# Optimization experiments

Measured on AMD Instinct MI355X. Metric: run time of the kernel, lower is better.

Reference implementation:

```python
import jax, jax.numpy as jnp
import numpy as np

D_MODEL = 1024
NUM_HEADS = 16
DEPTH = D_MODEL // NUM_HEADS


def setup_inputs() -> dict:
    key = jax.random.key(0)
    ks = jax.random.split(key, 9)
    B, S = 2, 2048
    scale = 1.0 / np.sqrt(D_MODEL)
    x = jax.random.normal(ks[0], (B, S, D_MODEL), dtype=jnp.float32)
    wq = jax.random.normal(ks[1], (D_MODEL, D_MODEL), dtype=jnp.float32) * scale
    bq = jax.random.normal(ks[2], (D_MODEL,), dtype=jnp.float32) * 0.01
    wk = jax.random.normal(ks[3], (D_MODEL, D_MODEL), dtype=jnp.float32) * scale
    bk = jax.random.normal(ks[4], (D_MODEL,), dtype=jnp.float32) * 0.01
    wv = jax.random.normal(ks[5], (D_MODEL, D_MODEL), dtype=jnp.float32) * scale
    bv = jax.random.normal(ks[6], (D_MODEL,), dtype=jnp.float32) * 0.01
    wo = jax.random.normal(ks[7], (D_MODEL, D_MODEL), dtype=jnp.float32) * scale
    bo = jax.random.normal(ks[8], (D_MODEL,), dtype=jnp.float32) * 0.01
    return {"x": x, "wq": wq, "bq": bq, "wk": wk, "bk": bk,
            "wv": wv, "bv": bv, "wo": wo, "bo": bo}


def reference(x, wq, bq, wk, bk, wv, bv, wo, bo):
    B, S, _ = x.shape
    def split_heads(t):  # [B,S,D] -> [B,H,S,depth]
        return t.reshape(B, S, NUM_HEADS, DEPTH).transpose(0, 2, 1, 3)
    q = split_heads(x @ wq + bq)
    k = split_heads(x @ wk + bk)
    v = split_heads(x @ wv + bv)
    # scaled dot-product attention, full [B,H,S,S] scores as in the original
    logits = jnp.einsum('bhqd,bhkd->bhqk', q, k) / jnp.sqrt(
        jnp.asarray(DEPTH, dtype=jnp.float32))
    attn = jax.nn.softmax(logits, axis=-1)
    out = jnp.einsum('bhqk,bhkd->bhqd', attn, v)
    out = out.transpose(0, 2, 1, 3).reshape(B, S, D_MODEL)
    return out @ wo + bo
```

## Files before the change

### kernel.cpp

```cpp
#include <hip/hip_runtime.h>


#define S_LEN 2048
#define DM 1024
#define MROWS 4096
#define QSCALE 0.1803368801111244f

typedef unsigned short u16;
typedef unsigned int u32;
typedef __attribute__((ext_vector_type(8))) short short8;
typedef __attribute__((ext_vector_type(4))) float f32x4;
typedef __attribute__((ext_vector_type(4))) unsigned short u16x4;

__device__ inline float bf2f(u16 h) {
    return __uint_as_float(((u32)h) << 16);
}
__device__ inline u16 f2bf(float f) {
    u32 u = __float_as_uint(f);
    u = u + 0x7fffu + ((u >> 16) & 1u);
    return (u16)(u >> 16);
}
__device__ inline float ldin(const void* p, size_t idx, int isf32) {
    return isf32 ? ((const float*)p)[idx] : bf2f(((const u16*)p)[idx]);
}
__device__ inline void gld_lds16(const u16* g, u16* l) {
    __builtin_amdgcn_global_load_lds(
        (const __attribute__((address_space(1))) void*)g,
        (__attribute__((address_space(3))) void*)l, 16, 0, 0);
}
__device__ inline f32x4 mfma16(short8 a, short8 b, f32x4 c) {
    return __builtin_amdgcn_mfma_f32_16x16x32_bf16(a, b, c, 0, 0, 0);
}

__global__ void init_flag(int* flag) { if (threadIdx.x == 0) *flag = 0; }

__global__ void detect_f32(const u16* __restrict__ x, int* flag) {
    const int idx = blockIdx.x * 256 + threadIdx.x;
    int bad = 0;
#pragma unroll
    for (int i = 0; i < 4; i++) {
        const u16 v = x[(size_t)idx * 4 + i];
        if ((v & 0x7F80u) == 0x7F80u) bad = 1;
    }
    if (bad) atomicOr(flag, 1);
}

__global__ void prep_all(const void* __restrict__ x, u16* __restrict__ xb,
                         const void* __restrict__ wq, const void* __restrict__ wk,
                         const void* __restrict__ wv, const void* __restrict__ wo,
                         const void* __restrict__ bq, const void* __restrict__ bk,
                         const void* __restrict__ bv, const void* __restrict__ bo,
                         u16* __restrict__ wallT, u16* __restrict__ woT,
                         float* __restrict__ biasAll, float* __restrict__ biasO,
                         const int* __restrict__ flag) {
    const int f = *flag;
    const int t = threadIdx.x;
    if (blockIdx.x < 2048) {
        const size_t i8 = ((size_t)blockIdx.x * 256 + t) * 8;
        if (f) {
            const f32x4 a = ((const f32x4*)x)[i8 / 4];
            const f32x4 b = ((const f32x4*)x)[i8 / 4 + 1];
            u16 o[8];
#pragma unroll
            for (int i = 0; i < 4; i++) { o[i] = f2bf(a[i]); o[4 + i] = f2bf(b[i]); }
            *(short8*)(xb + i8) = *(const short8*)o;
        } else {
            *(short8*)(xb + i8) = ((const short8*)x)[i8 / 8];
        }
        return;
    }
    const int bid = blockIdx.x - 2048;
    if (bid == 1024) {
#pragma unroll
        for (int i = 0; i < 4; i++) {
            const int idx = i * 256 + t;
            biasAll[idx]        = ldin(bq, idx, f) * QSCALE;
            biasAll[1024 + idx] = ldin(bk, idx, f);
            biasAll[2048 + idx] = ldin(bv, idx, f);
            biasO[idx]          = ldin(bo, idx, f);
        }
        return;
    }
    __shared__ float lds[64][65];
    const int m  = bid >> 8;
    const int tk = (bid >> 4) & 15;
    const int tn = bid & 15;
    const void* src = (m == 0) ? wq : (m == 1) ? wk : (m == 2) ? wv : wo;
    const float scale = (m == 0) ? QSCALE : 1.0f;
    const int r4 = t >> 6, c = t & 63;
#pragma unroll
    for (int i = 0; i < 16; i++) {
        const int k = tk * 64 + i * 4 + r4;
        lds[i * 4 + r4][c] = ldin(src, (size_t)k * 1024 + tn * 64 + c, f);
    }
    __syncthreads();
#pragma unroll
    for (int i = 0; i < 16; i++) {
        const int n = tn * 64 + i * 4 + r4;
        const int k = tk * 64 + c;
        const u16 v = f2bf(lds[c][i * 4 + r4] * scale);
        if (m < 3) wallT[((size_t)m * 1024 + n) * 1024 + k] = v;
        else       woT[(size_t)n * 1024 + k] = v;
    }
}

__global__ __launch_bounds__(256, 2)
void gemm_qkv(const u16* __restrict__ A, const u16* __restrict__ Bt,
              const float* __restrict__ bias, u16* __restrict__ Cq,
              u16* __restrict__ Ck, u16* __restrict__ Cv,
              const int K, const int N) {
    __shared__ __align__(16) u16 As[128 * 32];
    __shared__ __align__(16) u16 Bs[128 * 32];
    const int tid = threadIdx.x;
    const int w = tid >> 6, lane = tid & 63;
    const int wm = w >> 1, wn = w & 1;
    const int l16 = lane & 15, quad = lane >> 4;
    const int tm = blockIdx.x * 128;
    const int tn = blockIdx.y * 128;
    const int region = tn >> 10;

    const int sr = w * 16 + (lane >> 2);
    const int sc = (lane & 3) * 8;
    const u16* ag0 = A + (size_t)(tm + sr) * K + sc;
    const u16* ag1 = A + (size_t)(tm + sr + 64) * K + sc;
    const u16* bg0 = Bt + (size_t)(tn + sr) * K + sc;
    const u16* bg1 = Bt + (size_t)(tn + sr + 64) * K + sc;
    u16* al = As + w * 512;
    u16* bl = Bs + w * 512;

    f32x4 acc[4][4];
#pragma unroll
    for (int i = 0; i < 4; i++)
#pragma unroll
        for (int j = 0; j < 4; j++) acc[i][j] = (f32x4){0.f, 0.f, 0.f, 0.f};

    for (int kb = 0; kb < K; kb += 32) {
        __syncthreads();
        gld_lds16(ag0 + kb, al);
        gld_lds16(ag1 + kb, al + 2048);
        gld_lds16(bg0 + kb, bl);
        gld_lds16(bg1 + kb, bl + 2048);
        __syncthreads();
        short8 af[4], bfr[4];
#pragma unroll
        for (int i = 0; i < 4; i++) {
            af[i]  = *(const short8*)(As + (wm * 64 + i * 16 + l16) * 32 + quad * 8);
            bfr[i] = *(const short8*)(Bs + (wn * 64 + i * 16 + l16) * 32 + quad * 8);
        }
#pragma unroll
        for (int i = 0; i < 4; i++)
#pragma unroll
            for (int j = 0; j < 4; j++)
                acc[i][j] = mfma16(af[i], bfr[j], acc[i][j]);
    }
#pragma unroll
    for (int j = 0; j < 4; j++) {
        const int col = tn + wn * 64 + j * 16 + l16;
        const float bv = bias[col];
#pragma unroll
        for (int i = 0; i < 4; i++) {
            const int row0 = tm + wm * 64 + i * 16 + quad * 4;
#pragma unroll
            for (int r = 0; r < 4; r++) {
                const u16 vb = f2bf(acc[i][j][r] + bv);
                const int row = row0 + r;
                if (region == 0) {
                    Cq[(size_t)row * 1024 + col] = vb;
                } else if (region == 1) {
                    const int s = row & 2047, b = row >> 11;
                    const int hd = col - 1024, h = hd >> 6, d = hd & 63;
                    Ck[(((size_t)(b * 16 + h) * 2048 + s) << 6) +
                       (((d >> 3) + s) & 7) * 8 + (d & 7)] = vb;
                } else {
                    const int s = row & 2047, b = row >> 11;
                    const int hd = col - 2048, h = hd >> 6, d = hd & 63;
                    const int sl = s & 63;
                    const int p = (sl & 32) | ((sl & 15) << 1) | ((sl >> 4) & 1);
                    const int phys = ((((p >> 3) + d) & 7) << 3) | (p & 7);
                    Cv[(((size_t)((b * 16 + h) * 32 + (s >> 6))) << 12) +
                       d * 64 + phys] = vb;
                }
            }
        }
    }
}

__global__ __launch_bounds__(256, 2)
void gemm_out64(const u16* __restrict__ A, const u16* __restrict__ Bt,
                const float* __restrict__ bias, void* __restrict__ C,
                const int K, const int N, const int* __restrict__ flag) {
    __shared__ __align__(16) u16 As[64 * 32];
    __shared__ __align__(16) u16 Bs[128 * 32];
    const int tid = threadIdx.x;
    const int w = tid >> 6, lane = tid & 63;
    const int wm = w >> 1, wn = w & 1;
    const int l16 = lane & 15, quad = lane >> 4;
    const int tm = blockIdx.x * 64;
    const int tn = blockIdx.y * 128;
    const int outf = *flag;

    const int sr = w * 16 + (lane >> 2);
    const int sc = (lane & 3) * 8;
    const u16* ag  = A + (size_t)(tm + sr) * K + sc;
    const u16* bg0 = Bt + (size_t)(tn + sr) * K + sc;
    const u16* bg1 = Bt + (size_t)(tn + sr + 64) * K + sc;
    u16* al = As + w * 512;
    u16* bl = Bs + w * 512;

    f32x4 acc[2][4];
#pragma unroll
    for (int i = 0; i < 2; i++)
#pragma unroll
        for (int j = 0; j < 4; j++) acc[i][j] = (f32x4){0.f, 0.f, 0.f, 0.f};

    for (int kb = 0; kb < K; kb += 32) {
        __syncthreads();
        gld_lds16(ag + kb, al);
        gld_lds16(bg0 + kb, bl);
        gld_lds16(bg1 + kb, bl + 2048);
        __syncthreads();
        short8 af[2], bfr[4];
#pragma unroll
        for (int i = 0; i < 2; i++)
            af[i] = *(const short8*)(As + (wm * 32 + i * 16 + l16) * 32 + quad * 8);
#pragma unroll
        for (int j = 0; j < 4; j++)
            bfr[j] = *(const short8*)(Bs + (wn * 64 + j * 16 + l16) * 32 + quad * 8);
#pragma unroll
        for (int i = 0; i < 2; i++)
#pragma unroll
            for (int j = 0; j < 4; j++)
                acc[i][j] = mfma16(af[i], bfr[j], acc[i][j]);
    }
#pragma unroll
    for (int j = 0; j < 4; j++) {
        const int col = tn + wn * 64 + j * 16 + l16;
        const float bv = bias[col];
#pragma unroll
        for (int i = 0; i < 2; i++) {
            const int row0 = tm + wm * 32 + i * 16 + quad * 4;
#pragma unroll
            for (int r = 0; r < 4; r++) {
                const float val = acc[i][j][r] + bv;
                const size_t o = (size_t)(row0 + r) * N + col;
                if (outf) ((float*)C)[o] = val;
                else      ((u16*)C)[o]   = f2bf(val);
            }
        }
    }
}

__global__ __launch_bounds__(256, 2)
void flash_attn(const u16* __restrict__ Qb, const u16* __restrict__ Ktg,
                const u16* __restrict__ Vtb, u16* __restrict__ O) {
    __shared__ __align__(16) u16 Ks[4096];
    __shared__ __align__(16) u16 Vs[4096];
    const int tid = threadIdx.x;
    const int w = tid >> 6, lane = tid & 63;
    const int l16 = lane & 15, quad = lane >> 4;
    const int bh = blockIdx.y, b = bh >> 4, h = bh & 15;
    const int q0 = blockIdx.x * 128 + w * 32;

    short8 qf[2][2];
#pragma unroll
    for (int u = 0; u < 2; u++) {
        const size_t qrow = (size_t)(b * S_LEN + q0 + u * 16 + l16) * 1024 + h * 64;
        qf[u][0] = *(const short8*)(Qb + qrow + quad * 8);
        qf[u][1] = *(const short8*)(Qb + qrow + 32 + quad * 8);
    }

    const u16* kg = Ktg + ((size_t)bh << 17) + w * 1024 + lane * 8;
    const u16* vg = Vtb + ((size_t)bh << 17) + w * 1024 + lane * 8;
    u16* kl = Ks + w * 1024;
    u16* vl = Vs + w * 1024;

    const int ka0 = l16 * 64 + ((quad + l16) & 7) * 8;
    const int ka1 = l16 * 64 + ((4 + quad + l16) & 7) * 8;

    float lsum[2] = {0.f, 0.f};
    f32x4 o[2][4];
#pragma unroll
    for (int u = 0; u < 2; u++)
#pragma unroll
        for (int d = 0; d < 4; d++) o[u][d] = (f32x4){0.f, 0.f, 0.f, 0.f};
    const f32x4 zz = (f32x4){0.f, 0.f, 0.f, 0.f};

    for (int t = 0; t < S_LEN / 64; t++) {
        __syncthreads();
        gld_lds16(kg + t * 4096,       kl);
        gld_lds16(kg + t * 4096 + 512, kl + 512);
        gld_lds16(vg + t * 4096,       vl);
        gld_lds16(vg + t * 4096 + 512, vl + 512);
        __syncthreads();

        f32x4 s[2][4];
#pragma unroll
        for (int a = 0; a < 4; a++) {
            const short8 kf0 = *(const short8*)(Ks + a * 1024 + ka0);
            const short8 kf1 = *(const short8*)(Ks + a * 1024 + ka1);
#pragma unroll
            for (int u = 0; u < 2; u++) {
                s[u][a] = mfma16(kf0, qf[u][0], zz);
                s[u][a] = mfma16(kf1, qf[u][1], s[u][a]);
            }
        }
        union { u32 u[4]; short8 s8; } pu[2][2];
#pragma unroll
        for (int u = 0; u < 2; u++) {
#pragma unroll
            for (int r = 0; r < 4; r++) {
                const float e0 = __builtin_amdgcn_exp2f(s[u][0][r]);
                const float e1 = __builtin_amdgcn_exp2f(s[u][1][r]);
                const float e2 = __builtin_amdgcn_exp2f(s[u][2][r]);
                const float e3 = __builtin_amdgcn_exp2f(s[u][3][r]);
                lsum[u] += (e0 + e1) + (e2 + e3);
                pu[u][0].u[r] = __builtin_amdgcn_perm(
                    __float_as_uint(e1), __float_as_uint(e0), 0x07060302u);
                pu[u][1].u[r] = __builtin_amdgcn_perm(
                    __float_as_uint(e3), __float_as_uint(e2), 0x07060302u);
            }
        }
#pragma unroll
        for (int dv = 0; dv < 4; dv++) {
            const short8 vf0 = *(const short8*)(Vs + dv * 1024 + ka0);
            const short8 vf1 = *(const short8*)(Vs + dv * 1024 + ka1);
#pragma unroll
            for (int u = 0; u < 2; u++) {
                o[u][dv] = mfma16(vf0, pu[u][0].s8, o[u][dv]);
                o[u][dv] = mfma16(vf1, pu[u][1].s8, o[u][dv]);
            }
        }
    }

#pragma unroll
    for (int u = 0; u < 2; u++) {
        float ssum = lsum[u];
        ssum += __shfl_xor(ssum, 16);
        ssum += __shfl_xor(ssum, 32);
        const float inv = 1.0f / ssum;
        const size_t obase =
            (size_t)(b * S_LEN + q0 + u * 16 + l16) * DM + h * 64 + quad * 4;
#pragma unroll
        for (int d = 0; d < 4; d++) {
            u16x4 pk;
#pragma unroll
            for (int r = 0; r < 4; r++) pk[r] = f2bf(o[u][d][r] * inv);
            *(u16x4*)(O + obase + d * 16) = pk;
        }
    }
}

extern "C" void kernel_launch(void* const* d_in, const int* in_sizes, int n_in,
                              void* d_out, int out_size, void* d_ws, size_t ws_size,
                              hipStream_t stream) {
    const void* x  = d_in[0];
    const void* wq = d_in[1];
    const void* bq = d_in[2];
    const void* wk = d_in[3];
    const void* bk = d_in[4];
    const void* wv = d_in[5];
    const void* bv = d_in[6];
    const void* wo = d_in[7];
    const void* bo = d_in[8];

    char* ws = (char*)d_ws;
    int*   flag    = (int*)(ws + 0);
    u16*   wallT   = (u16*)(ws + 64);
    u16*   woT     = (u16*)(ws + 6291520);
    float* biasAll = (float*)(ws + 8388672);
    float* biasO   = (float*)(ws + 8400960);
    u16*   xb      = (u16*)(ws + 8405056);
    u16*   Qb      = (u16*)(ws + 16793664);
    u16*   Ktg     = (u16*)(ws + 25182272);
    u16*   Vtb     = (u16*)(ws + 33570880);
    u16*   Obuf    = (u16*)(ws + 41959488);

    init_flag<<<1, 64, 0, stream>>>(flag);
    detect_f32<<<256, 256, 0, stream>>>((const u16*)x, flag);
    prep_all<<<3073, 256, 0, stream>>>(x, xb, wq, wk, wv, wo, bq, bk, bv, bo,
                                       wallT, woT, biasAll, biasO, flag);
    gemm_qkv<<<dim3(32, 24), 256, 0, stream>>>(xb, wallT, biasAll,
                                               Qb, Ktg, Vtb, 1024, 3072);
    flash_attn<<<dim3(16, 32), 256, 0, stream>>>(Qb, Ktg, Vtb, Obuf);
    gemm_out64<<<dim3(64, 8), 256, 0, stream>>>(Obuf, woT, biasO, d_out,
                                                1024, 1024, flag);
}
```

Baseline: 203.9 us.

## Drop dtype detection, halve attention block size, compute row sums via MFMA

Removes the f32/bf16 detection kernels and flag branches, assuming float32 inputs and output. This drops two small launches and the per-element branches. The attention kernel now uses 128-thread blocks covering 64 queries with twice as many blocks, and each wave loads more of the shared K/V tile. The softmax denominator is computed by an MFMA against a ones vector instead of scalar adds plus cross-lane shuffles, which adds matrix work per tile but takes load off the VALU.

```diff
diff --git a/kernel.cpp b/kernel.cpp
--- a/kernel.cpp
+++ b/kernel.cpp
@@ -12,17 +12,11 @@
 typedef __attribute__((ext_vector_type(4))) float f32x4;
 typedef __attribute__((ext_vector_type(4))) unsigned short u16x4;
 
-__device__ inline float bf2f(u16 h) {
-    return __uint_as_float(((u32)h) << 16);
-}
 __device__ inline u16 f2bf(float f) {
     u32 u = __float_as_uint(f);
     u = u + 0x7fffu + ((u >> 16) & 1u);
     return (u16)(u >> 16);
 }
-__device__ inline float ldin(const void* p, size_t idx, int isf32) {
-    return isf32 ? ((const float*)p)[idx] : bf2f(((const u16*)p)[idx]);
-}
 __device__ inline void gld_lds16(const u16* g, u16* l) {
     __builtin_amdgcn_global_load_lds(
         (const __attribute__((address_space(1))) void*)g,
@@ -32,41 +26,22 @@
     return __builtin_amdgcn_mfma_f32_16x16x32_bf16(a, b, c, 0, 0, 0);
 }
 
-__global__ void init_flag(int* flag) { if (threadIdx.x == 0) *flag = 0; }
-
-__global__ void detect_f32(const u16* __restrict__ x, int* flag) {
-    const int idx = blockIdx.x * 256 + threadIdx.x;
-    int bad = 0;
-#pragma unroll
-    for (int i = 0; i < 4; i++) {
-        const u16 v = x[(size_t)idx * 4 + i];
-        if ((v & 0x7F80u) == 0x7F80u) bad = 1;
-    }
-    if (bad) atomicOr(flag, 1);
-}
-
-__global__ void prep_all(const void* __restrict__ x, u16* __restrict__ xb,
-                         const void* __restrict__ wq, const void* __restrict__ wk,
-                         const void* __restrict__ wv, const void* __restrict__ wo,
-                         const void* __restrict__ bq, const void* __restrict__ bk,
-                         const void* __restrict__ bv, const void* __restrict__ bo,
+__global__ void prep_all(const float* __restrict__ x, u16* __restrict__ xb,
+                         const float* __restrict__ wq, const float* __restrict__ wk,
+                         const float* __restrict__ wv, const float* __restrict__ wo,
+                         const float* __restrict__ bq, const float* __restrict__ bk,
+                         const float* __restrict__ bv, const float* __restrict__ bo,
                          u16* __restrict__ wallT, u16* __restrict__ woT,
-                         float* __restrict__ biasAll, float* __restrict__ biasO,
-                         const int* __restrict__ flag) {
-    const int f = *flag;
+                         float* __restrict__ biasAll, float* __restrict__ biasO) {
     const int t = threadIdx.x;
     if (blockIdx.x < 2048) {
         const size_t i8 = ((size_t)blockIdx.x * 256 + t) * 8;
-        if (f) {
-            const f32x4 a = ((const f32x4*)x)[i8 / 4];
-            const f32x4 b = ((const f32x4*)x)[i8 / 4 + 1];
-            u16 o[8];
-#pragma unroll
-            for (int i = 0; i < 4; i++) { o[i] = f2bf(a[i]); o[4 + i] = f2bf(b[i]); }
-            *(short8*)(xb + i8) = *(const short8*)o;
-        } else {
-            *(short8*)(xb + i8) = ((const short8*)x)[i8 / 8];
-        }
+        const f32x4 a = ((const f32x4*)x)[i8 / 4];
+        const f32x4 b = ((const f32x4*)x)[i8 / 4 + 1];
+        u16 o[8];
+#pragma unroll
+        for (int i = 0; i < 4; i++) { o[i] = f2bf(a[i]); o[4 + i] = f2bf(b[i]); }
+        *(short8*)(xb + i8) = *(const short8*)o;
         return;
     }
     const int bid = blockIdx.x - 2048;
@@ -74,10 +49,10 @@
 #pragma unroll
         for (int i = 0; i < 4; i++) {
             const int idx = i * 256 + t;
-            biasAll[idx]        = ldin(bq, idx, f) * QSCALE;
-            biasAll[1024 + idx] = ldin(bk, idx, f);
-            biasAll[2048 + idx] = ldin(bv, idx, f);
-            biasO[idx]          = ldin(bo, idx, f);
+            biasAll[idx]        = bq[idx] * QSCALE;
+            biasAll[1024 + idx] = bk[idx];
+            biasAll[2048 + idx] = bv[idx];
+            biasO[idx]          = bo[idx];
         }
         return;
     }
@@ -85,13 +60,13 @@
     const int m  = bid >> 8;
     const int tk = (bid >> 4) & 15;
     const int tn = bid & 15;
-    const void* src = (m == 0) ? wq : (m == 1) ? wk : (m == 2) ? wv : wo;
+    const float* src = (m == 0) ? wq : (m == 1) ? wk : (m == 2) ? wv : wo;
     const float scale = (m == 0) ? QSCALE : 1.0f;
     const int r4 = t >> 6, c = t & 63;
 #pragma unroll
     for (int i = 0; i < 16; i++) {
         const int k = tk * 64 + i * 4 + r4;
-        lds[i * 4 + r4][c] = ldin(src, (size_t)k * 1024 + tn * 64 + c, f);
+        lds[i * 4 + r4][c] = src[(size_t)k * 1024 + tn * 64 + c];
     }
     __syncthreads();
 #pragma unroll
@@ -187,8 +162,8 @@
 
 __global__ __launch_bounds__(256, 2)
 void gemm_out64(const u16* __restrict__ A, const u16* __restrict__ Bt,
-                const float* __restrict__ bias, void* __restrict__ C,
-                const int K, const int N, const int* __restrict__ flag) {
+                const float* __restrict__ bias, float* __restrict__ C,
+                const int K, const int N) {
     __shared__ __align__(16) u16 As[64 * 32];
     __shared__ __align__(16) u16 Bs[128 * 32];
     const int tid = threadIdx.x;
@@ -197,7 +172,6 @@
     const int l16 = lane & 15, quad = lane >> 4;
     const int tm = blockIdx.x * 64;
     const int tn = blockIdx.y * 128;
-    const int outf = *flag;
 
     const int sr = w * 16 + (lane >> 2);
     const int sc = (lane & 3) * 8;
@@ -240,17 +214,13 @@
         for (int i = 0; i < 2; i++) {
             const int row0 = tm + wm * 32 + i * 16 + quad * 4;
 #pragma unroll
-            for (int r = 0; r < 4; r++) {
-                const float val = acc[i][j][r] + bv;
-                const size_t o = (size_t)(row0 + r) * N + col;
-                if (outf) ((float*)C)[o] = val;
-                else      ((u16*)C)[o]   = f2bf(val);
-            }
-        }
-    }
-}
-
-__global__ __launch_bounds__(256, 2)
+            for (int r = 0; r < 4; r++)
+                C[(size_t)(row0 + r) * N + col] = acc[i][j][r] + bv;
+        }
+    }
+}
+
+__global__ __launch_bounds__(128, 2)
 void flash_attn(const u16* __restrict__ Qb, const u16* __restrict__ Ktg,
                 const u16* __restrict__ Vtb, u16* __restrict__ O) {
     __shared__ __align__(16) u16 Ks[4096];
@@ -259,7 +229,7 @@
     const int w = tid >> 6, lane = tid & 63;
     const int l16 = lane & 15, quad = lane >> 4;
     const int bh = blockIdx.y, b = bh >> 4, h = bh & 15;
-    const int q0 = blockIdx.x * 128 + w * 32;
+    const int q0 = blockIdx.x * 64 + w * 32;
 
     short8 qf[2][2];
 #pragma unroll
@@ -268,29 +238,39 @@
         qf[u][0] = *(const short8*)(Qb + qrow + quad * 8);
         qf[u][1] = *(const short8*)(Qb + qrow + 32 + quad * 8);
     }
-
-    const u16* kg = Ktg + ((size_t)bh << 17) + w * 1024 + lane * 8;
-    const u16* vg = Vtb + ((size_t)bh << 17) + w * 1024 + lane * 8;
-    u16* kl = Ks + w * 1024;
-    u16* vl = Vs + w * 1024;
+    u16 ones_s[8];
+#pragma unroll
+    for (int i = 0; i < 8; i++) ones_s[i] = 0x3F80u;
+    const short8 ones = *(const short8*)ones_s;
+
+    const u16* kg = Ktg + ((size_t)bh << 17) + w * 2048 + lane * 8;
+    const u16* vg = Vtb + ((size_t)bh << 17) + w * 2048 + lane * 8;
+    u16* kl = Ks + w * 2048;
+    u16* vl = Vs + w * 2048;
 
     const int ka0 = l16 * 64 + ((quad + l16) & 7) * 8;
     const int ka1 = l16 * 64 + ((4 + quad + l16) & 7) * 8;
 
-    float lsum[2] = {0.f, 0.f};
-    f32x4 o[2][4];
-#pragma unroll
-    for (int u = 0; u < 2; u++)
+    f32x4 o[2][4], osum[2];
+#pragma unroll
+    for (int u = 0; u < 2; u++) {
+        osum[u] = (f32x4){0.f, 0.f, 0.f, 0.f};
 #pragma unroll
         for (int d = 0; d < 4; d++) o[u][d] = (f32x4){0.f, 0.f, 0.f, 0.f};
+    }
     const f32x4 zz = (f32x4){0.f, 0.f, 0.f, 0.f};
 
     for (int t = 0; t < S_LEN / 64; t++) {
         __syncthreads();
-        gld_lds16(kg + t * 4096,       kl);
-        gld_lds16(kg + t * 4096 + 512, kl + 512);
-        gld_lds16(vg + t * 4096,       vl);
-        gld_lds16(vg + t * 4096 + 512, vl + 512);
+        const int off = t * 4096;
+        gld_lds16(kg + off,        kl);
+        gld_lds16(kg + off + 512,  kl + 512);
+        gld_lds16(kg + off + 1024, kl + 1024);
+        gld_lds16(kg + off + 1536, kl + 1536);
+        gld_lds16(vg + off,        vl);
+        gld_lds16(vg + off + 512,  vl + 512);
+        gld_lds16(vg + off + 1024, vl + 1024);
+        gld_lds16(vg + off + 1536, vl + 1536);
         __syncthreads();
 
         f32x4 s[2][4];
@@ -313,12 +293,13 @@
                 const float e1 = __builtin_amdgcn_exp2f(s[u][1][r]);
                 const float e2 = __builtin_amdgcn_exp2f(s[u][2][r]);
                 const float e3 = __builtin_amdgcn_exp2f(s[u][3][r]);
-                lsum[u] += (e0 + e1) + (e2 + e3);
                 pu[u][0].u[r] = __builtin_amdgcn_perm(
                     __float_as_uint(e1), __float_as_uint(e0), 0x07060302u);
                 pu[u][1].u[r] = __builtin_amdgcn_perm(
                     __float_as_uint(e3), __float_as_uint(e2), 0x07060302u);
             }
+            osum[u] = mfma16(ones, pu[u][0].s8, osum[u]);
+            osum[u] = mfma16(ones, pu[u][1].s8, osum[u]);
         }
 #pragma unroll
         for (int dv = 0; dv < 4; dv++) {
@@ -334,10 +315,7 @@
 
 #pragma unroll
     for (int u = 0; u < 2; u++) {
-        float ssum = lsum[u];
-        ssum += __shfl_xor(ssum, 16);
-        ssum += __shfl_xor(ssum, 32);
-        const float inv = 1.0f / ssum;
+        const float inv = 1.0f / osum[u][0];
         const size_t obase =
             (size_t)(b * S_LEN + q0 + u * 16 + l16) * DM + h * 64 + quad * 4;
 #pragma unroll
@@ -353,18 +331,17 @@
 extern "C" void kernel_launch(void* const* d_in, const int* in_sizes, int n_in,
                               void* d_out, int out_size, void* d_ws, size_t ws_size,
                               hipStream_t stream) {
-    const void* x  = d_in[0];
-    const void* wq = d_in[1];
-    const void* bq = d_in[2];
-    const void* wk = d_in[3];
-    const void* bk = d_in[4];
-    const void* wv = d_in[5];
-    const void* bv = d_in[6];
-    const void* wo = d_in[7];
-    const void* bo = d_in[8];
+    const float* x  = (const float*)d_in[0];
+    const float* wq = (const float*)d_in[1];
+    const float* bq = (const float*)d_in[2];
+    const float* wk = (const float*)d_in[3];
+    const float* bk = (const float*)d_in[4];
+    const float* wv = (const float*)d_in[5];
+    const float* bv = (const float*)d_in[6];
+    const float* wo = (const float*)d_in[7];
+    const float* bo = (const float*)d_in[8];
 
     char* ws = (char*)d_ws;
-    int*   flag    = (int*)(ws + 0);
     u16*   wallT   = (u16*)(ws + 64);
     u16*   woT     = (u16*)(ws + 6291520);
     float* biasAll = (float*)(ws + 8388672);
@@ -375,13 +352,11 @@
     u16*   Vtb     = (u16*)(ws + 33570880);
     u16*   Obuf    = (u16*)(ws + 41959488);
 
-    init_flag<<<1, 64, 0, stream>>>(flag);
-    detect_f32<<<256, 256, 0, stream>>>((const u16*)x, flag);
     prep_all<<<3073, 256, 0, stream>>>(x, xb, wq, wk, wv, wo, bq, bk, bv, bo,
-                                       wallT, woT, biasAll, biasO, flag);
+                                       wallT, woT, biasAll, biasO);
     gemm_qkv<<<dim3(32, 24), 256, 0, stream>>>(xb, wallT, biasAll,
                                                Qb, Ktg, Vtb, 1024, 3072);
-    flash_attn<<<dim3(16, 32), 256, 0, stream>>>(Qb, Ktg, Vtb, Obuf);
-    gemm_out64<<<dim3(64, 8), 256, 0, stream>>>(Obuf, woT, biasO, d_out,
-                                                1024, 1024, flag);
-}
+    flash_attn<<<dim3(32, 32), 128, 0, stream>>>(Qb, Ktg, Vtb, Obuf);
+    gemm_out64<<<dim3(64, 8), 256, 0, stream>>>(Obuf, woT, biasO,
+                                                (float*)d_out, 1024, 1024);
+}
```

After: 195.9 us. 3.9% less time.
